# Optimization experiments

Hardware: AMD Instinct MI355X
Metric: run time of the kernel (lower is better)

The kernel has to match this reference:

```python
import jax, jax.numpy as jnp
import numpy as np

T, B, H, L = 512, 32, 512, 2  # seq_len, batch, hidden_size, num_layers (input_size == H)


def _lstm_layer(x, Wih, Whh, bih, bhh):
    """x: [T,B,D]; Wih: [4H,D]; Whh: [4H,H]; biases: [4H]. Returns [T,B,H]."""
    # Precompute input contribution for all timesteps (one big GEMM).
    x_proj = jnp.einsum('tbd,gd->tbg', x, Wih) + bih + bhh  # [T,B,4H]
    h0 = jnp.zeros((x.shape[1], H), x.dtype)
    c0 = jnp.zeros((x.shape[1], H), x.dtype)

    def step(carry, xp):
        h, c = carry
        z = xp + h @ Whh.T  # [B,4H]
        i = jax.nn.sigmoid(z[:, 0 * H:1 * H])
        f = jax.nn.sigmoid(z[:, 1 * H:2 * H])
        g = jnp.tanh(z[:, 2 * H:3 * H])
        o = jax.nn.sigmoid(z[:, 3 * H:4 * H])
        c_new = f * c + i * g
        h_new = o * jnp.tanh(c_new)
        return (h_new, c_new), h_new

    (_, _), ys = jax.lax.scan(step, (h0, c0), x_proj)
    return ys  # [T,B,H]


def setup_inputs() -> dict:
    key = jax.random.key(0)
    k1, k2, k3, k4, k5 = jax.random.split(key, 5)
    scale = 1.0 / np.sqrt(H)  # torch Linear default init range ~ U(-1/sqrt(fan_in), ...)
    return {
        'seq_inputs': jax.random.normal(k1, (T, B, H), jnp.float32),
        'W_ih': jax.random.normal(k2, (L, 4 * H, H), jnp.float32) * scale,
        'W_hh': jax.random.normal(k3, (L, 4 * H, H), jnp.float32) * scale,
        'b_ih': jax.random.normal(k4, (L, 4 * H), jnp.float32) * scale,
        'b_hh': jax.random.normal(k5, (L, 4 * H), jnp.float32) * scale,
    }


def reference(seq_inputs, W_ih, W_hh, b_ih, b_hh):
    x = seq_inputs
    for l in range(L):  # small fixed layer loop
        x = _lstm_layer(x, W_ih[l], W_hh[l], b_ih[l], b_hh[l])
    return x  # [T,B,H] last-layer hidden sequence
```

## Files before the change

kernel.cpp:

```cpp
#include <hip/hip_runtime.h>


typedef _Float16 half8_t __attribute__((ext_vector_type(8)));
typedef _Float16 half4_t __attribute__((ext_vector_type(4)));
typedef float f32x4 __attribute__((ext_vector_type(4)));
typedef unsigned int u32;
typedef unsigned short u16;

#define T_LEN 512
#define BATCH 32
#define HID 512
#define SLOT 16384
#define LW (2048 * 512)

__device__ __forceinline__ float fast_sigmoid(float x) {
  return 1.f / (1.f + __expf(-x));
}
__device__ __forceinline__ float fast_tanh(float x) {
  return 1.f - 2.f / (1.f + __expf(2.f * x));
}

__device__ __forceinline__ void wait_flags(const u32* flags, int ln, u32 tgt, int self) {
  for (;;) {
    u32 v = __hip_atomic_load(flags + ln, __ATOMIC_RELAXED, __HIP_MEMORY_SCOPE_AGENT);
    if (__all((int)(v >= tgt) | (int)(ln == self))) break;
    __builtin_amdgcn_s_sleep(1);
  }
  asm volatile("" ::: "memory");
}

__global__ __launch_bounds__(256) void convert_k(
    const float4* __restrict__ x,
    const float4* __restrict__ wih,
    const float4* __restrict__ whh,
    const float* __restrict__ bih, const float* __restrict__ bhh,
    half4_t* __restrict__ xh, half4_t* __restrict__ wihh, half4_t* __restrict__ whhh,
    float* __restrict__ bsum) {
  const int N4X = 2097152, N4W = 524288, TOT = N4X + 2 * N4W;
  int gid = blockIdx.x * 256 + threadIdx.x;
  for (int i = gid; i < TOT; i += gridDim.x * 256) {
    float4 v;
    half4_t* dst;
    if (i < N4X) { v = x[i]; dst = xh + i; }
    else if (i < N4X + N4W) { v = wih[i - N4X]; dst = wihh + (i - N4X); }
    else { v = whh[i - N4X - N4W]; dst = whhh + (i - N4X - N4W); }
    half4_t h;
    h[0] = (_Float16)v.x; h[1] = (_Float16)v.y; h[2] = (_Float16)v.z; h[3] = (_Float16)v.w;
    *dst = h;
  }
  if (gid < 4096) bsum[gid] = bih[gid] + bhh[gid];
}

__global__ __launch_bounds__(128, 1) void lstm_fused(
    const _Float16* __restrict__ x0h,
    const _Float16* __restrict__ wih16,
    const _Float16* __restrict__ whh16,
    const float* __restrict__ bsum,
    _Float16* h0seq,
    _Float16* h1seq,
    u32* flags0, u32* flags1,
    float* outf) {
  int bid = blockIdx.x;
  int layer = bid >> 6, wg = bid & 63;
  int tid = threadIdx.x;
  int ln = tid & 63;
  int q = ln >> 4, l15 = ln & 15;
  int m0 = (tid >> 6) * 16;

  const _Float16* wih_l = wih16 + (size_t)layer * LW;
  const _Float16* whh_l = whh16 + (size_t)layer * LW;
  half8_t wx[2][16], wh[2][16];
  float bv[2];
#pragma unroll
  for (int j = 0; j < 2; ++j) {
    int nl = j * 16 + l15;
    int grow = (nl >> 3) * 512 + wg * 8 + (nl & 7);
    size_t ro = (size_t)grow * 512;
#pragma unroll
    for (int kc = 0; kc < 16; ++kc) {
      wx[j][kc] = *(const half8_t*)(wih_l + ro + kc * 32 + q * 8);
      wh[j][kc] = *(const half8_t*)(whh_l + ro + kc * 32 + q * 8);
    }
    bv[j] = bsum[layer * 2048 + grow];
  }

  const _Float16* xbase = layer ? (h0seq + SLOT) : x0h;
  _Float16* hself = layer ? h1seq : h0seq;
  u32* fself = layer ? flags1 : flags0;

  int cb = tid >> 2;
  int cp = tid & 3;
  int col0 = wg * 8 + cp * 2;
  float cst0 = 0.f, cst1 = 0.f;

  __shared__ float Zs[4 * 297];

  for (int t = 1; t <= T_LEN; ++t) {
    const _Float16* xsrc = xbase + (size_t)(t - 1) * SLOT;
    const _Float16* hsrc = hself + (size_t)(t - 1) * SLOT;
    f32x4 acc0 = {}, acc1 = {};
    half8_t af[16];

    if (layer == 0) {
#pragma unroll
      for (int kc = 0; kc < 16; ++kc)
        af[kc] = *(const half8_t*)(xsrc + (m0 + l15) * HID + kc * 32 + q * 8);
#pragma unroll
      for (int kc = 0; kc < 16; ++kc) {
        acc0 = __builtin_amdgcn_mfma_f32_16x16x32_f16(af[kc], wx[0][kc], acc0, 0, 0, 0);
        acc1 = __builtin_amdgcn_mfma_f32_16x16x32_f16(af[kc], wx[1][kc], acc1, 0, 0, 0);
      }
      if (t > 1) wait_flags(flags0, ln, (u32)(t - 1), wg);
#pragma unroll
      for (int kc = 0; kc < 16; ++kc)
        af[kc] = *(const half8_t*)(hsrc + (m0 + l15) * HID + kc * 32 + q * 8);
#pragma unroll
      for (int kc = 0; kc < 16; ++kc) {
        acc0 = __builtin_amdgcn_mfma_f32_16x16x32_f16(af[kc], wh[0][kc], acc0, 0, 0, 0);
        acc1 = __builtin_amdgcn_mfma_f32_16x16x32_f16(af[kc], wh[1][kc], acc1, 0, 0, 0);
      }
    } else {
      if (t > 1) wait_flags(flags1, ln, (u32)(t - 1), wg);
#pragma unroll
      for (int kc = 0; kc < 16; ++kc)
        af[kc] = *(const half8_t*)(hsrc + (m0 + l15) * HID + kc * 32 + q * 8);
#pragma unroll
      for (int kc = 0; kc < 16; ++kc) {
        acc0 = __builtin_amdgcn_mfma_f32_16x16x32_f16(af[kc], wh[0][kc], acc0, 0, 0, 0);
        acc1 = __builtin_amdgcn_mfma_f32_16x16x32_f16(af[kc], wh[1][kc], acc1, 0, 0, 0);
      }
      wait_flags(flags0, ln, (u32)t, -1);
#pragma unroll
      for (int kc = 0; kc < 16; ++kc)
        af[kc] = *(const half8_t*)(xsrc + (m0 + l15) * HID + kc * 32 + q * 8);
#pragma unroll
      for (int kc = 0; kc < 16; ++kc) {
        acc0 = __builtin_amdgcn_mfma_f32_16x16x32_f16(af[kc], wx[0][kc], acc0, 0, 0, 0);
        acc1 = __builtin_amdgcn_mfma_f32_16x16x32_f16(af[kc], wx[1][kc], acc1, 0, 0, 0);
      }
    }

#pragma unroll
    for (int j = 0; j < 2; ++j) {
      int nl = j * 16 + l15, g = nl >> 3, c = nl & 7;
      const f32x4& a = j ? acc1 : acc0;
#pragma unroll
      for (int r = 0; r < 4; ++r)
        Zs[g * 297 + (m0 + q * 4 + r) * 9 + c] = a[r] + bv[j];
    }
    __syncthreads();

    float h0, h1;
    {
      float zi0 = Zs[0 * 297 + cb * 9 + cp * 2], zi1 = Zs[0 * 297 + cb * 9 + cp * 2 + 1];
      float zf0 = Zs[1 * 297 + cb * 9 + cp * 2], zf1 = Zs[1 * 297 + cb * 9 + cp * 2 + 1];
      float zg0 = Zs[2 * 297 + cb * 9 + cp * 2], zg1 = Zs[2 * 297 + cb * 9 + cp * 2 + 1];
      float zo0 = Zs[3 * 297 + cb * 9 + cp * 2], zo1 = Zs[3 * 297 + cb * 9 + cp * 2 + 1];
      float i0 = fast_sigmoid(zi0), f0 = fast_sigmoid(zf0), g0 = fast_tanh(zg0), o0 = fast_sigmoid(zo0);
      float i1 = fast_sigmoid(zi1), f1 = fast_sigmoid(zf1), g1 = fast_tanh(zg1), o1 = fast_sigmoid(zo1);
      cst0 = f0 * cst0 + i0 * g0;
      cst1 = f1 * cst1 + i1 * g1;
      h0 = o0 * fast_tanh(cst0);
      h1 = o1 * fast_tanh(cst1);
      u32 hp = (u32)__builtin_bit_cast(u16, (_Float16)h0) |
               ((u32)__builtin_bit_cast(u16, (_Float16)h1) << 16);
      u32* hdst = (u32*)(hself + (size_t)t * SLOT + cb * HID + col0);
      __hip_atomic_store(hdst, hp, __ATOMIC_RELAXED, __HIP_MEMORY_SCOPE_AGENT);
    }
    __syncthreads();
    if (tid == 0)
      __hip_atomic_store(fself + wg, (u32)t, __ATOMIC_RELAXED, __HIP_MEMORY_SCOPE_AGENT);
    if (layer) {
      float2 o2; o2.x = h0; o2.y = h1;
      *(float2*)(outf + (size_t)(t - 1) * SLOT + cb * HID + col0) = o2;
    }
  }
}

extern "C" void kernel_launch(void* const* d_in, const int* in_sizes, int n_in,
                              void* d_out, int out_size, void* d_ws, size_t ws_size,
                              hipStream_t stream) {
  const float* x = (const float*)d_in[0];
  const float* Wih = (const float*)d_in[1];
  const float* Whh = (const float*)d_in[2];
  const float* bih = (const float*)d_in[3];
  const float* bhh = (const float*)d_in[4];
  char* ws = (char*)d_ws;
  const size_t OFF_X0H = 0;
  const size_t OFF_H0SEQ = 16777216;
  const size_t OFF_H1SEQ = 33587200;
  const size_t OFF_WIH = 50397184;
  const size_t OFF_WHH = 54591488;
  const size_t OFF_BSUM = 58785792;
  const size_t OFF_FLAGS0 = 58802176;
  const size_t OFF_FLAGS1 = 58802432;
  const size_t TOTAL = 58802688;
  if (ws_size < TOTAL) return;
  _Float16* x0h = (_Float16*)(ws + OFF_X0H);
  _Float16* h0seq = (_Float16*)(ws + OFF_H0SEQ);
  _Float16* h1seq = (_Float16*)(ws + OFF_H1SEQ);
  _Float16* wihh = (_Float16*)(ws + OFF_WIH);
  _Float16* whhh = (_Float16*)(ws + OFF_WHH);
  float* bsum = (float*)(ws + OFF_BSUM);
  u32* flags0 = (u32*)(ws + OFF_FLAGS0);
  u32* flags1 = (u32*)(ws + OFF_FLAGS1);

  hipMemsetAsync(ws + OFF_FLAGS0, 0, 512, stream);
  hipMemsetAsync(ws + OFF_H0SEQ, 0, 32768, stream);
  hipMemsetAsync(ws + OFF_H1SEQ, 0, 32768, stream);
  convert_k<<<3072, 256, 0, stream>>>((const float4*)x, (const float4*)Wih,
                                      (const float4*)Whh, bih, bhh,
                                      (half4_t*)x0h, (half4_t*)wihh, (half4_t*)whhh, bsum);
  lstm_fused<<<128, 128, 0, stream>>>(x0h, wihh, whhh, bsum, h0seq, h1seq,
                                      flags0, flags1, (float*)d_out);
}
```

Measured before the change: 3.316 ms.

## Replace per-step flag synchronization with canary-value polling on hidden-state data

Removes the per-workgroup flag array and its stores. Consumers now poll the hidden-state slots directly with atomic loads until no 32-bit word equals a canary pattern, which the convert kernel pre-fills into every future slot. This removes a flag round-trip (flag store, flag poll, then data load) from the serial recurrence's critical path. The cost is that the convert kernel must write canary data across both sequence buffers. Correctness also depends on no real fp16 pair ever equalling the canary bit pattern, and on the two 64-bit halves of each load being observed consistently.

```diff
diff --git a/kernel.cpp b/kernel.cpp
--- a/kernel.cpp
+++ b/kernel.cpp
@@ -5,13 +5,16 @@
 typedef _Float16 half4_t __attribute__((ext_vector_type(4)));
 typedef float f32x4 __attribute__((ext_vector_type(4)));
 typedef unsigned int u32;
+typedef u32 u32x4 __attribute__((ext_vector_type(4)));
 typedef unsigned short u16;
+typedef unsigned long long u64;
 
 #define T_LEN 512
 #define BATCH 32
 #define HID 512
 #define SLOT 16384
 #define LW (2048 * 512)
+#define CANARY 0x40404040u
 
 __device__ __forceinline__ float fast_sigmoid(float x) {
   return 1.f / (1.f + __expf(-x));
@@ -19,14 +22,26 @@
 __device__ __forceinline__ float fast_tanh(float x) {
   return 1.f - 2.f / (1.f + __expf(2.f * x));
 }
-
-__device__ __forceinline__ void wait_flags(const u32* flags, int ln, u32 tgt, int self) {
+__device__ __forceinline__ u32 umin_(u32 a, u32 b) { return a < b ? a : b; }
+
+__device__ __forceinline__ void poll_load_slot(const _Float16* src, int row, int q,
+                                               half8_t af[16]) {
+  const _Float16* base = src + row * HID + q * 8;
   for (;;) {
-    u32 v = __hip_atomic_load(flags + ln, __ATOMIC_RELAXED, __HIP_MEMORY_SCOPE_AGENT);
-    if (__all((int)(v >= tgt) | (int)(ln == self))) break;
+    u32 mn = 0xFFFFFFFFu;
+#pragma unroll
+    for (int kc = 0; kc < 16; ++kc) {
+      union { half8_t h; u64 q2[2]; u32 w[4]; } u;
+      const u64* p = (const u64*)(base + kc * 32);
+      u.q2[0] = __hip_atomic_load(p, __ATOMIC_RELAXED, __HIP_MEMORY_SCOPE_AGENT);
+      u.q2[1] = __hip_atomic_load(p + 1, __ATOMIC_RELAXED, __HIP_MEMORY_SCOPE_AGENT);
+      af[kc] = u.h;
+      mn = umin_(mn, umin_(umin_(u.w[0] ^ CANARY, u.w[1] ^ CANARY),
+                           umin_(u.w[2] ^ CANARY, u.w[3] ^ CANARY)));
+    }
+    if (__all(mn != 0)) break;
     __builtin_amdgcn_s_sleep(1);
   }
-  asm volatile("" ::: "memory");
 }
 
 __global__ __launch_bounds__(256) void convert_k(
@@ -35,10 +50,12 @@
     const float4* __restrict__ whh,
     const float* __restrict__ bih, const float* __restrict__ bhh,
     half4_t* __restrict__ xh, half4_t* __restrict__ wihh, half4_t* __restrict__ whhh,
-    float* __restrict__ bsum) {
+    float* __restrict__ bsum,
+    u32x4* __restrict__ h0fill, u32x4* __restrict__ h1fill) {
   const int N4X = 2097152, N4W = 524288, TOT = N4X + 2 * N4W;
   int gid = blockIdx.x * 256 + threadIdx.x;
-  for (int i = gid; i < TOT; i += gridDim.x * 256) {
+  int stride = gridDim.x * 256;
+  for (int i = gid; i < TOT; i += stride) {
     float4 v;
     half4_t* dst;
     if (i < N4X) { v = x[i]; dst = xh + i; }
@@ -48,6 +65,11 @@
     h[0] = (_Float16)v.x; h[1] = (_Float16)v.y; h[2] = (_Float16)v.z; h[3] = (_Float16)v.w;
     *dst = h;
   }
+  const int NF = 512 * (SLOT / 2) / 4;
+  u32x4 cv; cv[0] = CANARY; cv[1] = CANARY; cv[2] = CANARY; cv[3] = CANARY;
+  for (int i = gid; i < 2 * NF; i += stride) {
+    if (i < NF) h0fill[i] = cv; else h1fill[i - NF] = cv;
+  }
   if (gid < 4096) bsum[gid] = bih[gid] + bhh[gid];
 }
 
@@ -58,7 +80,6 @@
     const float* __restrict__ bsum,
     _Float16* h0seq,
     _Float16* h1seq,
-    u32* flags0, u32* flags1,
     float* outf) {
   int bid = blockIdx.x;
   int layer = bid >> 6, wg = bid & 63;
@@ -86,7 +107,6 @@
 
   const _Float16* xbase = layer ? (h0seq + SLOT) : x0h;
   _Float16* hself = layer ? h1seq : h0seq;
-  u32* fself = layer ? flags1 : flags0;
 
   int cb = tid >> 2;
   int cp = tid & 3;
@@ -110,29 +130,20 @@
         acc0 = __builtin_amdgcn_mfma_f32_16x16x32_f16(af[kc], wx[0][kc], acc0, 0, 0, 0);
         acc1 = __builtin_amdgcn_mfma_f32_16x16x32_f16(af[kc], wx[1][kc], acc1, 0, 0, 0);
       }
-      if (t > 1) wait_flags(flags0, ln, (u32)(t - 1), wg);
-#pragma unroll
-      for (int kc = 0; kc < 16; ++kc)
-        af[kc] = *(const half8_t*)(hsrc + (m0 + l15) * HID + kc * 32 + q * 8);
+      poll_load_slot(hsrc, m0 + l15, q, af);
 #pragma unroll
       for (int kc = 0; kc < 16; ++kc) {
         acc0 = __builtin_amdgcn_mfma_f32_16x16x32_f16(af[kc], wh[0][kc], acc0, 0, 0, 0);
         acc1 = __builtin_amdgcn_mfma_f32_16x16x32_f16(af[kc], wh[1][kc], acc1, 0, 0, 0);
       }
     } else {
-      if (t > 1) wait_flags(flags1, ln, (u32)(t - 1), wg);
-#pragma unroll
-      for (int kc = 0; kc < 16; ++kc)
-        af[kc] = *(const half8_t*)(hsrc + (m0 + l15) * HID + kc * 32 + q * 8);
+      poll_load_slot(hsrc, m0 + l15, q, af);
 #pragma unroll
       for (int kc = 0; kc < 16; ++kc) {
         acc0 = __builtin_amdgcn_mfma_f32_16x16x32_f16(af[kc], wh[0][kc], acc0, 0, 0, 0);
         acc1 = __builtin_amdgcn_mfma_f32_16x16x32_f16(af[kc], wh[1][kc], acc1, 0, 0, 0);
       }
-      wait_flags(flags0, ln, (u32)t, -1);
-#pragma unroll
-      for (int kc = 0; kc < 16; ++kc)
-        af[kc] = *(const half8_t*)(xsrc + (m0 + l15) * HID + kc * 32 + q * 8);
+      poll_load_slot(xsrc, m0 + l15, q, af);
 #pragma unroll
       for (int kc = 0; kc < 16; ++kc) {
         acc0 = __builtin_amdgcn_mfma_f32_16x16x32_f16(af[kc], wx[0][kc], acc0, 0, 0, 0);
@@ -168,8 +179,6 @@
       __hip_atomic_store(hdst, hp, __ATOMIC_RELAXED, __HIP_MEMORY_SCOPE_AGENT);
     }
     __syncthreads();
-    if (tid == 0)
-      __hip_atomic_store(fself + wg, (u32)t, __ATOMIC_RELAXED, __HIP_MEMORY_SCOPE_AGENT);
     if (layer) {
       float2 o2; o2.x = h0; o2.y = h1;
       *(float2*)(outf + (size_t)(t - 1) * SLOT + cb * HID + col0) = o2;
@@ -192,8 +201,6 @@
   const size_t OFF_WIH = 50397184;
   const size_t OFF_WHH = 54591488;
   const size_t OFF_BSUM = 58785792;
-  const size_t OFF_FLAGS0 = 58802176;
-  const size_t OFF_FLAGS1 = 58802432;
   const size_t TOTAL = 58802688;
   if (ws_size < TOTAL) return;
   _Float16* x0h = (_Float16*)(ws + OFF_X0H);
@@ -202,15 +209,13 @@
   _Float16* wihh = (_Float16*)(ws + OFF_WIH);
   _Float16* whhh = (_Float16*)(ws + OFF_WHH);
   float* bsum = (float*)(ws + OFF_BSUM);
-  u32* flags0 = (u32*)(ws + OFF_FLAGS0);
-  u32* flags1 = (u32*)(ws + OFF_FLAGS1);
-
-  hipMemsetAsync(ws + OFF_FLAGS0, 0, 512, stream);
+
   hipMemsetAsync(ws + OFF_H0SEQ, 0, 32768, stream);
   hipMemsetAsync(ws + OFF_H1SEQ, 0, 32768, stream);
   convert_k<<<3072, 256, 0, stream>>>((const float4*)x, (const float4*)Wih,
                                       (const float4*)Whh, bih, bhh,
-                                      (half4_t*)x0h, (half4_t*)wihh, (half4_t*)whhh, bsum);
+                                      (half4_t*)x0h, (half4_t*)wihh, (half4_t*)whhh, bsum,
+                                      (u32x4*)(h0seq + SLOT), (u32x4*)(h1seq + SLOT));
   lstm_fused<<<128, 128, 0, stream>>>(x0h, wihh, whhh, bsum, h0seq, h1seq,
-                                      flags0, flags1, (float*)d_out);
-}
+                                      (float*)d_out);
+}
```

Result: slower. 5.858 ms (+76.6%).
